# Kernel optimization log

Hardware: AMD Instinct MI355X
Metric: run time of the kernel (lower is better)

The kernel has to match this reference:

```python
import jax, jax.numpy as jnp
import numpy as np

DIM = 2048   # token width; == heads*head_dim
H, DH = 16, 128
B, S = 1, 2048
E, K = 4, 2          # routed experts, top-k
HID = 5632           # per-expert SwiGLU hidden: round256(int(2*(4*DIM)/3))
HS = 2816            # shared expert hidden: round256(int(2*(2*DIM)/3))


def setup_inputs() -> dict:
    key = jax.random.key(0)
    ks = jax.random.split(key, 24)
    def g(i, shape, s=0.02):
        return jax.random.normal(ks[i], shape, dtype=jnp.float32) * s
    return {
        "image_tokens": jax.random.normal(ks[0], (B, S, DIM), dtype=jnp.float32),
        "adaln_input": jax.random.normal(ks[1], (B, DIM), dtype=jnp.float32),
        "W_ada": g(2, (DIM, 6 * DIM)), "b_ada": g(3, (6 * DIM,)),
        "Wq": g(4, (DIM, DIM)), "bq": g(5, (DIM,)),
        "Wk": g(6, (DIM, DIM)), "bk": g(7, (DIM,)),
        "Wv": g(8, (DIM, DIM)), "bv": g(9, (DIM,)),
        "q_rms_w": jnp.ones((DIM,), jnp.float32) + g(10, (DIM,)),
        "k_rms_w": jnp.ones((DIM,), jnp.float32) + g(11, (DIM,)),
        "Wo": g(12, (DIM, DIM)), "bo": g(13, (DIM,)),
        "gate_w": g(14, (E, DIM)),
        "We1": g(15, (E, DIM, HID)), "We3": g(16, (E, DIM, HID)), "We2": g(17, (E, HID, DIM)),
        "Ws1": g(18, (DIM, HS)), "Ws3": g(19, (DIM, HS)), "Ws2": g(20, (HS, DIM)),
    }


def _ln(x):  # LayerNorm, elementwise_affine=False, eps=1e-6
    m = jnp.mean(x, -1, keepdims=True)
    v = jnp.var(x, -1, keepdims=True)
    return (x - m) * jax.lax.rsqrt(v + 1e-6)


def _rms(x, w):  # RMSNorm with affine weight, eps=1e-5
    return x * jax.lax.rsqrt(jnp.mean(x * x, -1, keepdims=True) + 1e-5) * w


def reference(image_tokens, adaln_input, W_ada, b_ada, Wq, bq, Wk, bk, Wv, bv,
              q_rms_w, k_rms_w, Wo, bo, gate_w, We1, We3, We2, Ws1, Ws3, Ws2):
    # adaLN: SiLU -> Linear -> 6 chunks, each broadcast as [B,1,dim]
    mod = (jax.nn.silu(adaln_input) @ W_ada + b_ada)[:, None, :]
    sh_msa, sc_msa, g_msa, sh_mlp, sc_mlp, g_mlp = jnp.split(mod, 6, axis=-1)

    # attention branch
    x = _ln(image_tokens) * (1.0 + sc_msa) + sh_msa
    q = _rms(x @ Wq + bq, q_rms_w).reshape(B, S, H, DH)
    k = _rms(x @ Wk + bk, k_rms_w).reshape(B, S, H, DH)
    v = (x @ Wv + bv).reshape(B, S, H, DH)
    att = jax.nn.softmax(jnp.einsum('bihd,bjhd->bhij', q, k) / jnp.sqrt(jnp.float32(DH)), axis=-1)
    o = jnp.einsum('bhij,bjhd->bihd', att, v).reshape(B, S, DIM) @ Wo + bo
    img = g_msa * o + image_tokens

    # MoE SwiGLU FFN branch
    y = _ln(img) * (1.0 + sc_mlp) + sh_mlp
    xf = y.reshape(-1, DIM)                                   # [N, dim]
    scores = jax.nn.softmax(xf @ gate_w.T, axis=-1)           # [N, E]
    tw, ti = jax.lax.top_k(scores, K)                         # no top-k renorm (norm_topk_prob=False)
    comb = jnp.zeros((xf.shape[0], E), xf.dtype).at[jnp.arange(xf.shape[0])[:, None], ti].add(tw)
    h = jax.nn.silu(jnp.einsum('nd,edh->neh', xf, We1)) * jnp.einsum('nd,edh->neh', xf, We3)
    routed = jnp.einsum('neh,ehd,ne->nd', h, We2, comb)
    shared = (jax.nn.silu(xf @ Ws1) * (xf @ Ws3)) @ Ws2
    ff = (routed + shared).reshape(B, S, DIM)

    return g_mlp * ff + img
```

## Files before the change

kernel.cpp:

```cpp
#include <hip/hip_runtime.h>
#include <hip/hip_bf16.h>

typedef unsigned short u16;
typedef __bf16 bf16x8 __attribute__((ext_vector_type(8)));
typedef float f32x4 __attribute__((ext_vector_type(4)));
typedef unsigned short u16x8 __attribute__((ext_vector_type(8)));

constexpr int DIMC = 2048;
constexpr int SEQ = 2048;
constexpr int NHEAD = 16;
constexpr int HDIM = 128;
constexpr int NEXP = 4;
constexpr int HIDC = 5632;
constexpr int HSH = 2816;
constexpr int MOD6 = 6 * DIMC;
constexpr int RSTRIDE = 2304;

static __device__ __forceinline__ u16 f2bf(float f) {
  __hip_bfloat16 b = __float2bfloat16(f);
  return __builtin_bit_cast(u16, b);
}
static __device__ __forceinline__ float bf2f(u16 u) {
  unsigned int x = ((unsigned int)u) << 16;
  return __builtin_bit_cast(float, x);
}
static __device__ __forceinline__ float sigf(float x) { return 1.f / (1.f + __expf(-x)); }

static __device__ __forceinline__ void gload16(const void* src, void* dst) {
  __builtin_amdgcn_global_load_lds((const __attribute__((address_space(1))) void*)src,
                                   (__attribute__((address_space(3))) void*)dst, 16, 0, 0);
}

static __device__ __forceinline__ void split44(f32x4 lo, f32x4 hi, bf16x8& h, bf16x8& l) {
#pragma unroll
  for (int e = 0; e < 4; ++e) {
    float f0 = lo[e];
    u16 h0 = f2bf(f0);
    h[e] = __builtin_bit_cast(__bf16, h0);
    l[e] = __builtin_bit_cast(__bf16, f2bf(f0 - bf2f(h0)));
    float f1 = hi[e];
    u16 h1 = f2bf(f1);
    h[4 + e] = __builtin_bit_cast(__bf16, h1);
    l[4 + e] = __builtin_bit_cast(__bf16, f2bf(f1 - bf2f(h1)));
  }
}

static __device__ __forceinline__ float blockSum(float v) {
#pragma unroll
  for (int m = 1; m < 64; m <<= 1) v += __shfl_xor(v, m);
  __shared__ float s[4];
  int w = threadIdx.x >> 6;
  if ((threadIdx.x & 63) == 0) s[w] = v;
  __syncthreads();
  float r = s[0] + s[1] + s[2] + s[3];
  __syncthreads();
  return r;
}

__global__ __launch_bounds__(256) void k_transpose(const float* __restrict__ in, u16* __restrict__ out,
                                                   int R, int C, int ldin, size_t inz, size_t outz) {
  __shared__ __align__(16) float tile[32][33];
  const float* inp = in + (size_t)blockIdx.z * inz;
  u16* outp = out + (size_t)blockIdx.z * outz;
  int tx = threadIdx.x & 31, ty = threadIdx.x >> 5;
  int c0 = blockIdx.x * 32, r0 = blockIdx.y * 32;
#pragma unroll
  for (int i = 0; i < 32; i += 8)
    tile[ty + i][tx] = inp[(size_t)(r0 + ty + i) * ldin + c0 + tx];
  __syncthreads();
#pragma unroll
  for (int i = 0; i < 32; i += 8)
    outp[(size_t)(c0 + ty + i) * R + r0 + tx] = f2bf(tile[tx][ty + i]);
}

__global__ __launch_bounds__(256) void k_transpose_f(const float* __restrict__ in, float* __restrict__ out,
                                                     int R, int C, int ldin) {
  __shared__ __align__(16) float tile[32][33];
  int tx = threadIdx.x & 31, ty = threadIdx.x >> 5;
  int c0 = blockIdx.x * 32, r0 = blockIdx.y * 32;
#pragma unroll
  for (int i = 0; i < 32; i += 8)
    tile[ty + i][tx] = in[(size_t)(r0 + ty + i) * ldin + c0 + tx];
  __syncthreads();
#pragma unroll
  for (int i = 0; i < 32; i += 8)
    out[(size_t)(c0 + ty + i) * R + r0 + tx] = tile[tx][ty + i];
}

__global__ __launch_bounds__(256) void k_adaln_p(const float* __restrict__ a, const float* __restrict__ W,
                                                 float* __restrict__ partial) {
  __shared__ float sa[128];
  int tid = threadIdx.x, slice = blockIdx.y;
  if (tid < 128) { float v = a[slice * 128 + tid]; sa[tid] = v * sigf(v); }
  __syncthreads();
  int j = blockIdx.x * 256 + tid;
  float acc = 0.f;
#pragma unroll 4
  for (int d = 0; d < 128; ++d) acc += sa[d] * W[(size_t)(slice * 128 + d) * MOD6 + j];
  partial[(size_t)slice * MOD6 + j] = acc;
}
__global__ __launch_bounds__(256) void k_adaln_r(const float* __restrict__ partial, const float* __restrict__ b,
                                                 float* __restrict__ mod) {
  int j = blockIdx.x * 256 + threadIdx.x;
  float acc = b[j];
#pragma unroll
  for (int s = 0; s < 16; ++s) acc += partial[(size_t)s * MOD6 + j];
  mod[j] = acc;
}

__global__ __launch_bounds__(256) void k_ln_modf(const float* __restrict__ X, const float* __restrict__ mod,
                                                 int shOff, int scOff, float* __restrict__ out) {
  int row = blockIdx.x, tid = threadIdx.x;
  const float4* x4 = (const float4*)(X + (size_t)row * DIMC);
  float4 v0 = x4[tid * 2], v1 = x4[tid * 2 + 1];
  float s = v0.x + v0.y + v0.z + v0.w + v1.x + v1.y + v1.z + v1.w;
  float ss = v0.x * v0.x + v0.y * v0.y + v0.z * v0.z + v0.w * v0.w +
             v1.x * v1.x + v1.y * v1.y + v1.z * v1.z + v1.w * v1.w;
  s = blockSum(s);
  ss = blockSum(ss);
  float mean = s * (1.f / DIMC);
  float var = ss * (1.f / DIMC) - mean * mean;
  float rstd = rsqrtf(var + 1e-6f);
  const float* sh = mod + shOff;
  const float* sc = mod + scOff;
  int c = tid * 8;
  float xv[8] = {v0.x, v0.y, v0.z, v0.w, v1.x, v1.y, v1.z, v1.w};
  float ov[8];
#pragma unroll
  for (int e = 0; e < 8; ++e) ov[e] = (xv[e] - mean) * rstd * (1.f + sc[c + e]) + sh[c + e];
  float4 o0 = {ov[0], ov[1], ov[2], ov[3]}, o1 = {ov[4], ov[5], ov[6], ov[7]};
  float4* y4 = (float4*)(out + (size_t)row * DIMC);
  y4[tid * 2] = o0;
  y4[tid * 2 + 1] = o1;
}

__global__ __launch_bounds__(256) void k_ln_mod(const float* __restrict__ X, const float* __restrict__ mod,
                                                int shOff, int scOff, u16* __restrict__ out) {
  int row = blockIdx.x, tid = threadIdx.x;
  const float4* x4 = (const float4*)(X + (size_t)row * DIMC);
  float4 v0 = x4[tid * 2], v1 = x4[tid * 2 + 1];
  float s = v0.x + v0.y + v0.z + v0.w + v1.x + v1.y + v1.z + v1.w;
  float ss = v0.x * v0.x + v0.y * v0.y + v0.z * v0.z + v0.w * v0.w +
             v1.x * v1.x + v1.y * v1.y + v1.z * v1.z + v1.w * v1.w;
  s = blockSum(s);
  ss = blockSum(ss);
  float mean = s * (1.f / DIMC);
  float var = ss * (1.f / DIMC) - mean * mean;
  float rstd = rsqrtf(var + 1e-6f);
  const float* sh = mod + shOff;
  const float* sc = mod + scOff;
  int c = tid * 8;
  float xv[8] = {v0.x, v0.y, v0.z, v0.w, v1.x, v1.y, v1.z, v1.w};
  u16x8 o;
#pragma unroll
  for (int e = 0; e < 8; ++e) o[e] = f2bf((xv[e] - mean) * rstd * (1.f + sc[c + e]) + sh[c + e]);
  *(u16x8*)(out + (size_t)row * DIMC + c) = o;
}

__global__ __launch_bounds__(256) void k_rms_f32(const float* __restrict__ X, const float* __restrict__ w,
                                                 float scale, float* __restrict__ out) {
  int row = blockIdx.x, tid = threadIdx.x;
  const float4* x4 = (const float4*)(X + (size_t)row * DIMC);
  float4 v0 = x4[tid * 2], v1 = x4[tid * 2 + 1];
  float ss = v0.x * v0.x + v0.y * v0.y + v0.z * v0.z + v0.w * v0.w +
             v1.x * v1.x + v1.y * v1.y + v1.z * v1.z + v1.w * v1.w;
  ss = blockSum(ss);
  float rstd = rsqrtf(ss * (1.f / DIMC) + 1e-5f) * scale;
  int c = tid * 8;
  float xv[8] = {v0.x, v0.y, v0.z, v0.w, v1.x, v1.y, v1.z, v1.w};
  float ov[8];
#pragma unroll
  for (int e = 0; e < 8; ++e) ov[e] = xv[e] * rstd * w[c + e];
  float4 o0 = {ov[0], ov[1], ov[2], ov[3]}, o1 = {ov[4], ov[5], ov[6], ov[7]};
  float4* y4 = (float4*)(out + (size_t)row * DIMC);
  y4[tid * 2] = o0;
  y4[tid * 2 + 1] = o1;
}

__global__ __launch_bounds__(256) void k_gate(const float* __restrict__ img, const float* __restrict__ mod,
                                              const float* __restrict__ gw, float* __restrict__ comb) {
  int n = blockIdx.x, tid = threadIdx.x;
  const float4* x4 = (const float4*)(img + (size_t)n * DIMC);
  float4 v0 = x4[tid * 2], v1 = x4[tid * 2 + 1];
  float s = v0.x + v0.y + v0.z + v0.w + v1.x + v1.y + v1.z + v1.w;
  float ss = v0.x * v0.x + v0.y * v0.y + v0.z * v0.z + v0.w * v0.w +
             v1.x * v1.x + v1.y * v1.y + v1.z * v1.z + v1.w * v1.w;
  s = blockSum(s);
  ss = blockSum(ss);
  float mean = s * (1.f / DIMC);
  float var = ss * (1.f / DIMC) - mean * mean;
  float rstd = rsqrtf(var + 1e-6f);
  const float* sh = mod + 3 * DIMC;
  const float* sc = mod + 4 * DIMC;
  int c = tid * 8;
  float xv[8] = {v0.x, v0.y, v0.z, v0.w, v1.x, v1.y, v1.z, v1.w};
  float y[8];
#pragma unroll
  for (int e = 0; e < 8; ++e) y[e] = (xv[e] - mean) * rstd * (1.f + sc[c + e]) + sh[c + e];
  float accs[NEXP];
#pragma unroll
  for (int ex = 0; ex < NEXP; ++ex) {
    float a = 0.f;
#pragma unroll
    for (int e = 0; e < 8; ++e) a += y[e] * gw[(size_t)ex * DIMC + c + e];
    accs[ex] = blockSum(a);
  }
  if (tid == 0) {
    float mx = fmaxf(fmaxf(accs[0], accs[1]), fmaxf(accs[2], accs[3]));
    float ex0 = __expf(accs[0] - mx), ex1 = __expf(accs[1] - mx);
    float ex2 = __expf(accs[2] - mx), ex3 = __expf(accs[3] - mx);
    float inv = 1.f / (ex0 + ex1 + ex2 + ex3);
    float v[4] = {ex0 * inv, ex1 * inv, ex2 * inv, ex3 * inv};
    int i1 = 0;
    for (int e = 1; e < 4; ++e)
      if (v[e] > v[i1]) i1 = e;
    int i2 = -1;
    for (int e = 0; e < 4; ++e) {
      if (e == i1) continue;
      if (i2 < 0 || v[e] > v[i2]) i2 = e;
    }
    for (int e = 0; e < 4; ++e) comb[(size_t)n * 4 + e] = (e == i1 || e == i2) ? v[e] : 0.f;
  }
}

__global__ __launch_bounds__(256) void k_route(const float* __restrict__ comb, int* __restrict__ gidx,
                                               float* __restrict__ cw, int* __restrict__ Mpad) {
  int wid = threadIdx.x >> 6, lane = threadIdx.x & 63;
  int base = 0;
  for (int c = 0; c < SEQ; c += 64) {
    int n = c + lane;
    float w = comb[(size_t)n * NEXP + wid];
    bool sel = w > 0.f;
    unsigned long long mask = __ballot(sel);
    int pos = __popcll(mask & ((1ull << lane) - 1ull));
    if (sel) {
      gidx[wid * RSTRIDE + base + pos] = n;
      cw[wid * RSTRIDE + base + pos] = w;
    }
    base += __popcll(mask);
  }
  int padded = (base + 127) & ~127;
  for (int i = base + lane; i < padded; i += 64) {
    gidx[wid * RSTRIDE + i] = -1;
    cw[wid * RSTRIDE + i] = 0.f;
  }
  if (lane == 0) Mpad[wid] = padded;
}

template <int MODE>
__global__ __launch_bounds__(256, 2) void k_gemm(const u16* __restrict__ A, const u16* __restrict__ BT,
                                                 int M, int N, int K, float* __restrict__ Cf,
                                                 u16* __restrict__ Cb, const u16* __restrict__ h1) {
  __shared__ __align__(16) u16 AsA[4096], AsB[4096], BsA[4096], BsB[4096];
  const int tid = threadIdx.x, wid = tid >> 6, lane = tid & 63;
  const int l16 = lane & 15, g = lane >> 4;
  const int wr = wid >> 1, wc = wid & 1;
  const int m0 = blockIdx.y * 128, n0 = blockIdx.x * 128;
  const int srow = lane >> 2, scol = (lane & 3) * 8;
  const u16* aS0 = A + (size_t)(m0 + wid * 32 + srow) * K + scol;
// ... 100 lines not shown
    row0 = slot0;
    row1 = slot0 + 16;
  } else {
    int t0 = gidxE[slot0], t1 = gidxE[slot0 + 16];
    row0 = t0 < 0 ? 0 : t0;
    row1 = t1 < 0 ? 0 : t1;
  }
  const u16* aS0 = A + (size_t)row0 * K + scol;
  const u16* aS1 = A + (size_t)row1 * K + scol;
  const u16* bS0 = BT + (size_t)(n0 + wid * 32 + srow) * K + scol;
  const u16* bS1 = bS0 + (size_t)16 * K;
  u16* aDA0 = &AsA[wid * 1024];
  u16* aDA1 = aDA0 + 512;
  u16* bDA0 = &BsA[wid * 1024];
  u16* bDA1 = bDA0 + 512;
  u16* aDB0 = &AsB[wid * 1024];
  u16* aDB1 = aDB0 + 512;
  u16* bDB0 = &BsB[wid * 1024];
  u16* bDB1 = bDB0 + 512;

  const f32x4 zero4 = {0.f, 0.f, 0.f, 0.f};
  f32x4 acc[4][4];
#pragma unroll
  for (int mi = 0; mi < 4; ++mi)
#pragma unroll
    for (int ni = 0; ni < 4; ++ni) acc[mi][ni] = zero4;

  for (int k0 = 0; k0 < K; k0 += 64) {
    __syncthreads();
    gload16(aS0 + k0, aDA0);
    gload16(aS1 + k0, aDA1);
    gload16(bS0 + k0, bDA0);
    gload16(bS1 + k0, bDA1);
    gload16(aS0 + k0 + 32, aDB0);
    gload16(aS1 + k0 + 32, aDB1);
    gload16(bS0 + k0 + 32, bDB0);
    gload16(bS1 + k0 + 32, bDB1);
    __syncthreads();
#pragma unroll
    for (int hh = 0; hh < 2; ++hh) {
      const u16* Asrc = hh ? AsB : AsA;
      const u16* Bsrc = hh ? BsB : BsA;
      bf16x8 af[4], bfr[4];
#pragma unroll
      for (int mi = 0; mi < 4; ++mi)
        af[mi] = *(const bf16x8*)(&Asrc[(wr * 64 + mi * 16 + l16) * 32 + g * 8]);
#pragma unroll
      for (int ni = 0; ni < 4; ++ni)
        bfr[ni] = *(const bf16x8*)(&Bsrc[(wc * 64 + ni * 16 + l16) * 32 + g * 8]);
#pragma unroll
      for (int mi = 0; mi < 4; ++mi)
#pragma unroll
        for (int ni = 0; ni < 4; ++ni)
          acc[mi][ni] = __builtin_amdgcn_mfma_f32_16x16x32_bf16(af[mi], bfr[ni], acc[mi][ni], 0, 0, 0);
    }
  }

#pragma unroll
  for (int mi = 0; mi < 4; ++mi) {
#pragma unroll
    for (int ni = 0; ni < 4; ++ni) {
      const int col = n0 + wc * 64 + ni * 16 + l16;
#pragma unroll
      for (int r = 0; r < 4; ++r) {
        const int slot = m0 + wr * 64 + mi * 16 + g * 4 + r;
        const size_t idx = (size_t)slot * N + col;
        float v = acc[mi][ni][r];
        if constexpr (RM == 0) {
          Cb[idx] = f2bf(v);
        } else if constexpr (RM == 1) {
          float hv = bf2f(h1[idx]);
          float sw = hv * sigf(hv);
          Cb[idx] = f2bf(sw * v * cwE[slot]);
        } else {
          int t = gidxE[slot];
          if (t >= 0) ff[(size_t)t * N + col] += v;
        }
      }
    }
  }
}

template <int MODE>
__global__ __launch_bounds__(256, 2) void k_gemm3(const float* __restrict__ A, const float* __restrict__ BT,
                                                  int M, int N, int K, float* __restrict__ Cf,
                                                  const float* __restrict__ bias,
                                                  const float* __restrict__ gvec,
                                                  const float* __restrict__ resid) {
  __shared__ __align__(16) u16 Ah[128 * 40], Al[128 * 40], Bh[128 * 40], Bl[128 * 40];
  const int tid = threadIdx.x, wid = tid >> 6, lane = tid & 63;
  const int l16 = lane & 15, g = lane >> 4;
  const int wr = wid >> 1, wc = wid & 1;
  const int m0 = blockIdx.y * 128, n0 = blockIdx.x * 128;

  const int srow = tid >> 1, se0 = (tid & 1) * 16;
  char* ahp = (char*)Ah + srow * 80 + se0 * 2;
  char* alp = (char*)Al + srow * 80 + se0 * 2;
  char* bhp = (char*)Bh + srow * 80 + se0 * 2;
  char* blp = (char*)Bl + srow * 80 + se0 * 2;
  const float* aS = A + (size_t)(m0 + srow) * K + se0;
  const float* bS = BT + (size_t)(n0 + srow) * K + se0;

  f32x4 ar[4], br[4];
#pragma unroll
  for (int c = 0; c < 4; ++c) {
    ar[c] = *(const f32x4*)(aS + c * 4);
    br[c] = *(const f32x4*)(bS + c * 4);
  }

  const f32x4 zero4 = {0.f, 0.f, 0.f, 0.f};
  f32x4 acc[4][4];
#pragma unroll
  for (int mi = 0; mi < 4; ++mi)
#pragma unroll
    for (int ni = 0; ni < 4; ++ni) acc[mi][ni] = zero4;

  for (int k0 = 0; k0 < K; k0 += 32) {
    __syncthreads();
    bf16x8 h0, l0, h1, l1;
    split44(ar[0], ar[1], h0, l0);
    split44(ar[2], ar[3], h1, l1);
    *(bf16x8*)(ahp) = h0;
    *(bf16x8*)(ahp + 16) = h1;
    *(bf16x8*)(alp) = l0;
    *(bf16x8*)(alp + 16) = l1;
    split44(br[0], br[1], h0, l0);
    split44(br[2], br[3], h1, l1);
    *(bf16x8*)(bhp) = h0;
    *(bf16x8*)(bhp + 16) = h1;
    *(bf16x8*)(blp) = l0;
    *(bf16x8*)(blp + 16) = l1;
    __syncthreads();
    if (k0 + 32 < K) {
#pragma unroll
      for (int c = 0; c < 4; ++c) {
        ar[c] = *(const f32x4*)(aS + k0 + 32 + c * 4);
        br[c] = *(const f32x4*)(bS + k0 + 32 + c * 4);
      }
    }
    bf16x8 bhf[4], blf[4];
#pragma unroll
    for (int ni = 0; ni < 4; ++ni) {
      const int rb = wc * 64 + ni * 16 + l16;
      bhf[ni] = *(const bf16x8*)((char*)Bh + rb * 80 + g * 16);
      blf[ni] = *(const bf16x8*)((char*)Bl + rb * 80 + g * 16);
    }
#pragma unroll
    for (int mi = 0; mi < 4; ++mi) {
      const int ra = wr * 64 + mi * 16 + l16;
      bf16x8 ahf = *(const bf16x8*)((char*)Ah + ra * 80 + g * 16);
      bf16x8 alf = *(const bf16x8*)((char*)Al + ra * 80 + g * 16);
#pragma unroll
      for (int ni = 0; ni < 4; ++ni) {
        acc[mi][ni] = __builtin_amdgcn_mfma_f32_16x16x32_bf16(alf, bhf[ni], acc[mi][ni], 0, 0, 0);
        acc[mi][ni] = __builtin_amdgcn_mfma_f32_16x16x32_bf16(ahf, blf[ni], acc[mi][ni], 0, 0, 0);
        acc[mi][ni] = __builtin_amdgcn_mfma_f32_16x16x32_bf16(ahf, bhf[ni], acc[mi][ni], 0, 0, 0);
      }
    }
  }

#pragma unroll
  for (int mi = 0; mi < 4; ++mi) {
#pragma unroll
    for (int ni = 0; ni < 4; ++ni) {
      const int col = n0 + wc * 64 + ni * 16 + l16;
      float bv = bias ? bias[col] : 0.f;
#pragma unroll
      for (int r = 0; r < 4; ++r) {
        const int row = m0 + wr * 64 + mi * 16 + g * 4 + r;
        float v = acc[mi][ni][r] + bv;
        if constexpr (MODE == 0) {
          Cf[(size_t)row * N + col] = v;
        } else if constexpr (MODE == 2) {
          Cf[(size_t)row * N + col] = v * gvec[col] + resid[(size_t)row * N + col];
        } else {
          Cf[(size_t)col * M + row] = v;
        }
      }
    }
  }
}

__global__ __launch_bounds__(256, 2) void k_flash3(const float* __restrict__ q, const float* __restrict__ kk,
                                                   const float* __restrict__ vt, float* __restrict__ o) {
  __shared__ __align__(16) u16 Kh[4096], Kl[4096], Vh[128 * 40], Vl[128 * 40];
  __shared__ __align__(16) u16 Pah[4][16 * 40], Pal[4][16 * 40];
  const int tid = threadIdx.x, wid = tid >> 6, lane = tid & 63;
  const int l16 = lane & 15, g = lane >> 4;
  const int h = blockIdx.y;
  const int r0 = blockIdx.x * 64 + wid * 16;
  const size_t hOff = (size_t)h * HDIM;

  bf16x8 qh[4], ql[4];
#pragma unroll
  for (int kc = 0; kc < 4; ++kc) {
    const float* qp = q + (size_t)(r0 + l16) * DIMC + hOff + kc * 32 + g * 8;
    split44(*(const f32x4*)qp, *(const f32x4*)(qp + 4), qh[kc], ql[kc]);
  }

  const int kr = tid >> 3, ke0 = (tid & 7) * 16;
  const int kswz = (kr & 7) << 4;
  const int kc0 = (ke0 * 2) ^ kswz, kc1 = (ke0 * 2 + 16) ^ kswz;
  char* khp = (char*)Kh + kr * 256;
  char* klp = (char*)Kl + kr * 256;
  const float* kBase = kk + (size_t)kr * DIMC + hOff + ke0;
  const int vr = tid >> 1, ve0 = (tid & 1) * 16;
  char* vhp = (char*)Vh + vr * 80 + ve0 * 2;
  char* vlp = (char*)Vl + vr * 80 + ve0 * 2;
  const float* vBase = vt + (size_t)(hOff + vr) * SEQ + ve0;

  f32x4 kReg[4], vReg[4];
#pragma unroll
  for (int c = 0; c < 4; ++c) {
    kReg[c] = *(const f32x4*)(kBase + c * 4);
    vReg[c] = *(const f32x4*)(vBase + c * 4);
  }

  const f32x4 zero4 = {0.f, 0.f, 0.f, 0.f};
  f32x4 oacc[8];
#pragma unroll
  for (int db = 0; db < 8; ++db) oacc[db] = zero4;
  float mr[4], lr[4];
#pragma unroll
  for (int r = 0; r < 4; ++r) {
    mr[r] = -3.0e38f;
    lr[r] = 0.f;
  }

  for (int j0 = 0; j0 < SEQ; j0 += 32) {
    __syncthreads();
    bf16x8 h0, l0, h1, l1;
    split44(kReg[0], kReg[1], h0, l0);
    split44(kReg[2], kReg[3], h1, l1);
    *(bf16x8*)(khp + kc0) = h0;
    *(bf16x8*)(khp + kc1) = h1;
    *(bf16x8*)(klp + kc0) = l0;
    *(bf16x8*)(klp + kc1) = l1;
    split44(vReg[0], vReg[1], h0, l0);
    split44(vReg[2], vReg[3], h1, l1);
    *(bf16x8*)(vhp) = h0;
    *(bf16x8*)(vhp + 16) = h1;
    *(bf16x8*)(vlp) = l0;
    *(bf16x8*)(vlp + 16) = l1;
    __syncthreads();
    if (j0 + 32 < SEQ) {
      const float* kp = kBase + (size_t)(j0 + 32) * DIMC;
      const float* vp = vBase + j0 + 32;
#pragma unroll
      for (int c = 0; c < 4; ++c) {
        kReg[c] = *(const f32x4*)(kp + c * 4);
        vReg[c] = *(const f32x4*)(vp + c * 4);
      }
    }
    f32x4 s0 = zero4, s1 = zero4;
    __builtin_amdgcn_s_setprio(1);
#pragma unroll
    for (int kc = 0; kc < 4; ++kc) {
      const int cb = (kc * 64 + g * 16) ^ ((l16 & 7) << 4);
      bf16x8 kh0 = *(const bf16x8*)((char*)Kh + l16 * 256 + cb);
      bf16x8 kl0 = *(const bf16x8*)((char*)Kl + l16 * 256 + cb);
      bf16x8 kh1 = *(const bf16x8*)((char*)Kh + (16 + l16) * 256 + cb);
      bf16x8 kl1 = *(const bf16x8*)((char*)Kl + (16 + l16) * 256 + cb);
      s0 = __builtin_amdgcn_mfma_f32_16x16x32_bf16(ql[kc], kh0, s0, 0, 0, 0);
      s0 = __builtin_amdgcn_mfma_f32_16x16x32_bf16(qh[kc], kl0, s0, 0, 0, 0);
      s0 = __builtin_amdgcn_mfma_f32_16x16x32_bf16(qh[kc], kh0, s0, 0, 0, 0);
      s1 = __builtin_amdgcn_mfma_f32_16x16x32_bf16(ql[kc], kh1, s1, 0, 0, 0);
      s1 = __builtin_amdgcn_mfma_f32_16x16x32_bf16(qh[kc], kl1, s1, 0, 0, 0);
      s1 = __builtin_amdgcn_mfma_f32_16x16x32_bf16(qh[kc], kh1, s1, 0, 0, 0);
    }
    __builtin_amdgcn_s_setprio(0);
    float corr[4];
#pragma unroll
    for (int r = 0; r < 4; ++r) {
      float tm = fmaxf(s0[r], s1[r]);
#pragma unroll
      for (int m = 1; m < 16; m <<= 1) tm = fmaxf(tm, __shfl_xor(tm, m));
      float mn = fmaxf(mr[r], tm);
      corr[r] = __expf(mr[r] - mn);
      mr[r] = mn;
      float p0 = __expf(s0[r] - mn);
      float p1 = __expf(s1[r] - mn);
      lr[r] = lr[r] * corr[r] + p0 + p1;
      u16 p0h = f2bf(p0), p1h = f2bf(p1);
      Pah[wid][(g * 4 + r) * 40 + l16] = p0h;
      Pah[wid][(g * 4 + r) * 40 + 16 + l16] = p1h;
      Pal[wid][(g * 4 + r) * 40 + l16] = f2bf(p0 - bf2f(p0h));
      Pal[wid][(g * 4 + r) * 40 + 16 + l16] = f2bf(p1 - bf2f(p1h));
    }
#pragma unroll
    for (int db = 0; db < 8; ++db)
#pragma unroll
      for (int r = 0; r < 4; ++r) oacc[db][r] *= corr[r];
    bf16x8 pfh = *(const bf16x8*)(&Pah[wid][l16 * 40 + g * 8]);
    bf16x8 pfl = *(const bf16x8*)(&Pal[wid][l16 * 40 + g * 8]);
    __builtin_amdgcn_s_setprio(1);
#pragma unroll
    for (int db = 0; db < 8; ++db) {
      const int row = db * 16 + l16;
      bf16x8 vh = *(const bf16x8*)((char*)Vh + row * 80 + g * 16);
      bf16x8 vl = *(const bf16x8*)((char*)Vl + row * 80 + g * 16);
      oacc[db] = __builtin_amdgcn_mfma_f32_16x16x32_bf16(pfl, vh, oacc[db], 0, 0, 0);
      oacc[db] = __builtin_amdgcn_mfma_f32_16x16x32_bf16(pfh, vl, oacc[db], 0, 0, 0);
      oacc[db] = __builtin_amdgcn_mfma_f32_16x16x32_bf16(pfh, vh, oacc[db], 0, 0, 0);
    }
    __builtin_amdgcn_s_setprio(0);
  }
#pragma unroll
  for (int r = 0; r < 4; ++r) {
#pragma unroll
    for (int m = 1; m < 16; m <<= 1) lr[r] += __shfl_xor(lr[r], m);
    lr[r] = 1.f / lr[r];
  }
#pragma unroll
  for (int db = 0; db < 8; ++db)
#pragma unroll
    for (int r = 0; r < 4; ++r)
      o[(size_t)(r0 + g * 4 + r) * DIMC + hOff + db * 16 + l16] = oacc[db][r] * lr[r];
}

__global__ __launch_bounds__(256) void k_final(const float* __restrict__ ff, const float* img,
                                               const float* __restrict__ mod, float* out) {
  const float4* gm = (const float4*)(mod + 5 * DIMC);
  const int total = SEQ * DIMC / 4;
  const int stride = gridDim.x * blockDim.x;
  for (int i = blockIdx.x * blockDim.x + threadIdx.x; i < total; i += stride) {
    int col4 = i & (DIMC / 4 - 1);
    float4 gv = gm[col4];
    float4 fv = ((const float4*)ff)[i];
    float4 iv = ((const float4*)img)[i];
    float4 ov;
    ov.x = gv.x * fv.x + iv.x;
    ov.y = gv.y * fv.y + iv.y;
    ov.z = gv.z * fv.z + iv.z;
    ov.w = gv.w * fv.w + iv.w;
    ((float4*)out)[i] = ov;
  }
}

extern "C" void kernel_launch(void* const* d_in, const int* in_sizes, int n_in, void* d_out, int out_size,
                              void* d_ws, size_t ws_size, hipStream_t stream) {
  (void)in_sizes; (void)n_in; (void)out_size; (void)ws_size;
  const float* image_tokens = (const float*)d_in[0];
  const float* adaln_input = (const float*)d_in[1];
  const float* W_ada = (const float*)d_in[2];
  const float* b_ada = (const float*)d_in[3];
  const float* Wq = (const float*)d_in[4];
  const float* bq = (const float*)d_in[5];
  const float* Wk = (const float*)d_in[6];
  const float* bk = (const float*)d_in[7];
  const float* Wv = (const float*)d_in[8];
  const float* bv = (const float*)d_in[9];
  const float* q_rms_w = (const float*)d_in[10];
  const float* k_rms_w = (const float*)d_in[11];
  const float* Wo = (const float*)d_in[12];
  const float* bo = (const float*)d_in[13];
  const float* gate_w = (const float*)d_in[14];
  const float* We1 = (const float*)d_in[15];
  const float* We3 = (const float*)d_in[16];
  const float* We2 = (const float*)d_in[17];
  const float* Ws1 = (const float*)d_in[18];
  const float* Ws3 = (const float*)d_in[19];
  const float* Ws2 = (const float*)d_in[20];

  char* cur = (char*)d_ws;
  auto alloc = [&](size_t n) {
    char* p = cur;
    cur += (n + 255) & ~(size_t)255;
    return p;
  };
  float* modv = (float*)alloc((size_t)MOD6 * 4);
  float* adap = (float*)alloc((size_t)16 * MOD6 * 4);
  float* comb = (float*)alloc((size_t)SEQ * NEXP * 4);
  int* gidx = (int*)alloc((size_t)NEXP * RSTRIDE * 4);
  float* cw = (float*)alloc((size_t)NEXP * RSTRIDE * 4);
  int* Mpad = (int*)alloc((size_t)NEXP * 4);
  float* xf = (float*)alloc((size_t)SEQ * DIMC * 4);
  float* wTf = (float*)alloc((size_t)DIMC * DIMC * 4);
  float* tf = (float*)alloc((size_t)SEQ * DIMC * 4);
  float* qf = (float*)alloc((size_t)SEQ * DIMC * 4);
  float* kf = (float*)alloc((size_t)SEQ * DIMC * 4);
  float* vtf = (float*)alloc((size_t)SEQ * DIMC * 4);
  float* aof = (float*)alloc((size_t)SEQ * DIMC * 4);
  u16* x_act = (u16*)alloc((size_t)SEQ * DIMC * 2);
  float* ff = (float*)alloc((size_t)SEQ * DIMC * 4);
  float* img = (float*)d_out;
  u16* wbufE = (u16*)xf;
  u16* H1G2 = (u16*)((char*)xf + (size_t)2 * HIDC * DIMC * 2);
  const size_t BZ = (size_t)HIDC * DIMC;
  const size_t CZ = (size_t)RSTRIDE * HIDC;
  u16* wbufS = wbufE;
  u16* H1Gs = H1G2;

  dim3 blk(256);
  auto gemm3 = [&](int mode, const float* A, const float* BT, int M, int N, int K, float* Cf,
                   const float* bias, const float* gv, const float* resid) {
    dim3 grid(N / 128, M / 128);
    switch (mode) {
      case 0: k_gemm3<0><<<grid, blk, 0, stream>>>(A, BT, M, N, K, Cf, bias, gv, resid); break;
      case 2: k_gemm3<2><<<grid, blk, 0, stream>>>(A, BT, M, N, K, Cf, bias, gv, resid); break;
      default: k_gemm3<6><<<grid, blk, 0, stream>>>(A, BT, M, N, K, Cf, bias, gv, resid); break;
    }
  };

  k_adaln_p<<<dim3(MOD6 / 256, 16), blk, 0, stream>>>(adaln_input, W_ada, adap);
  k_adaln_r<<<dim3(MOD6 / 256), blk, 0, stream>>>(adap, b_ada, modv);

  k_ln_modf<<<dim3(SEQ), blk, 0, stream>>>(image_tokens, modv, 0, DIMC, xf);
  k_transpose_f<<<dim3(DIMC / 32, DIMC / 32), blk, 0, stream>>>(Wq, wTf, DIMC, DIMC, DIMC);
  gemm3(0, xf, wTf, SEQ, DIMC, DIMC, tf, bq, nullptr, nullptr);
  k_rms_f32<<<dim3(SEQ), blk, 0, stream>>>(tf, q_rms_w, 0.08838834764831845f, qf);
  k_transpose_f<<<dim3(DIMC / 32, DIMC / 32), blk, 0, stream>>>(Wk, wTf, DIMC, DIMC, DIMC);
  gemm3(0, xf, wTf, SEQ, DIMC, DIMC, tf, bk, nullptr, nullptr);
  k_rms_f32<<<dim3(SEQ), blk, 0, stream>>>(tf, k_rms_w, 1.f, kf);
  k_transpose_f<<<dim3(DIMC / 32, DIMC / 32), blk, 0, stream>>>(Wv, wTf, DIMC, DIMC, DIMC);
  gemm3(6, xf, wTf, SEQ, DIMC, DIMC, vtf, bv, nullptr, nullptr);
  k_flash3<<<dim3(SEQ / 64, NHEAD), blk, 0, stream>>>(qf, kf, vtf, aof);
  k_transpose_f<<<dim3(DIMC / 32, DIMC / 32), blk, 0, stream>>>(Wo, wTf, DIMC, DIMC, DIMC);
  gemm3(2, aof, wTf, SEQ, DIMC, DIMC, img, bo, modv + 2 * DIMC, image_tokens);

  k_ln_mod<<<dim3(SEQ), blk, 0, stream>>>(img, modv, 3 * DIMC, 4 * DIMC, x_act);
  k_gate<<<dim3(SEQ), blk, 0, stream>>>(img, modv, gate_w, comb);
  k_route<<<dim3(1), blk, 0, stream>>>(comb, gidx, cw, Mpad);

  k_transpose<<<dim3(HSH / 32, DIMC / 32), blk, 0, stream>>>(Ws1, wbufS, DIMC, HSH, HSH, 0, 0);
  k_gemm<1><<<dim3(HSH / 128, SEQ / 128), blk, 0, stream>>>(x_act, wbufS, SEQ, HSH, DIMC, nullptr,
                                                            H1Gs, nullptr);
  k_transpose<<<dim3(HSH / 32, DIMC / 32), blk, 0, stream>>>(Ws3, wbufS, DIMC, HSH, HSH, 0, 0);
  k_gemm<3><<<dim3(HSH / 128, SEQ / 128), blk, 0, stream>>>(x_act, wbufS, SEQ, HSH, DIMC, nullptr,
                                                            H1Gs, H1Gs);
  k_transpose<<<dim3(DIMC / 32, HSH / 32), blk, 0, stream>>>(Ws2, wbufS, HSH, DIMC, DIMC, 0, 0);
  k_gemm<0><<<dim3(DIMC / 128, SEQ / 128), blk, 0, stream>>>(H1Gs, wbufS, SEQ, DIMC, HSH, ff,
                                                             nullptr, nullptr);

  const size_t WE = (size_t)DIMC * HIDC;
  for (int p = 0; p < 2; ++p) {
    const int e0 = p * 2;
    const int* ge = gidx + e0 * RSTRIDE;
    const float* ce = cw + e0 * RSTRIDE;
    const int* me = Mpad + e0;
    k_transpose<<<dim3(HIDC / 32, DIMC / 32, 2), blk, 0, stream>>>(We1 + (size_t)e0 * WE, wbufE,
                                                                   DIMC, HIDC, HIDC, WE, BZ);
    k_gemmR<0><<<dim3(HIDC / 128, SEQ / 128, 2), blk, 0, stream>>>(x_act, 0, wbufE, BZ, HIDC, DIMC,
                                                                   ge, ce, me, H1G2, CZ, H1G2, nullptr);
    k_transpose<<<dim3(HIDC / 32, DIMC / 32, 2), blk, 0, stream>>>(We3 + (size_t)e0 * WE, wbufE,
                                                                   DIMC, HIDC, HIDC, WE, BZ);
    k_gemmR<1><<<dim3(HIDC / 128, SEQ / 128, 2), blk, 0, stream>>>(x_act, 0, wbufE, BZ, HIDC, DIMC,
                                                                   ge, ce, me, H1G2, CZ, H1G2, nullptr);
    k_transpose<<<dim3(DIMC / 32, HIDC / 32, 2), blk, 0, stream>>>(We2 + (size_t)e0 * WE, wbufE,
                                                                   HIDC, DIMC, DIMC, WE, BZ);
    for (int z = 0; z < 2; ++z) {
      k_gemmR<2><<<dim3(DIMC / 128, SEQ / 128, 1), blk, 0, stream>>>(
          H1G2 + (size_t)z * CZ, 0, wbufE + (size_t)z * BZ, 0, DIMC, HIDC, gidx + (e0 + z) * RSTRIDE,
          cw + (e0 + z) * RSTRIDE, Mpad + e0 + z, H1G2, 0, H1G2, ff);
    }
  }

  k_final<<<dim3(1024), blk, 0, stream>>>(ff, img, modv, (float*)d_out);
}
```

Measured before the change: 1.694 ms.

## Pre-split fp32 operands into bf16 hi/lo pairs in producer kernels for attention GEMMs

```diff
diff --git a/kernel.cpp b/kernel.cpp
--- a/kernel.cpp
+++ b/kernel.cpp
@@ -25,24 +25,14 @@
   return __builtin_bit_cast(float, x);
 }
 static __device__ __forceinline__ float sigf(float x) { return 1.f / (1.f + __expf(-x)); }
+static __device__ __forceinline__ void splitf(float f, u16& h, u16& l) {
+  h = f2bf(f);
+  l = f2bf(f - bf2f(h));
+}
 
 static __device__ __forceinline__ void gload16(const void* src, void* dst) {
   __builtin_amdgcn_global_load_lds((const __attribute__((address_space(1))) void*)src,
                                    (__attribute__((address_space(3))) void*)dst, 16, 0, 0);
-}
-
-static __device__ __forceinline__ void split44(f32x4 lo, f32x4 hi, bf16x8& h, bf16x8& l) {
-#pragma unroll
-  for (int e = 0; e < 4; ++e) {
-    float f0 = lo[e];
-    u16 h0 = f2bf(f0);
-    h[e] = __builtin_bit_cast(__bf16, h0);
-    l[e] = __builtin_bit_cast(__bf16, f2bf(f0 - bf2f(h0)));
-    float f1 = hi[e];
-    u16 h1 = f2bf(f1);
-    h[4 + e] = __builtin_bit_cast(__bf16, h1);
-    l[4 + e] = __builtin_bit_cast(__bf16, f2bf(f1 - bf2f(h1)));
-  }
 }
 
 static __device__ __forceinline__ float blockSum(float v) {
@@ -73,8 +63,8 @@
     outp[(size_t)(c0 + ty + i) * R + r0 + tx] = f2bf(tile[tx][ty + i]);
 }
 
-__global__ __launch_bounds__(256) void k_transpose_f(const float* __restrict__ in, float* __restrict__ out,
-                                                     int R, int C, int ldin) {
+__global__ __launch_bounds__(256) void k_transpose_s(const float* __restrict__ in, u16* __restrict__ outh,
+                                                     u16* __restrict__ outl, int R, int C, int ldin) {
   __shared__ __align__(16) float tile[32][33];
   int tx = threadIdx.x & 31, ty = threadIdx.x >> 5;
   int c0 = blockIdx.x * 32, r0 = blockIdx.y * 32;
@@ -83,8 +73,14 @@
     tile[ty + i][tx] = in[(size_t)(r0 + ty + i) * ldin + c0 + tx];
   __syncthreads();
 #pragma unroll
-  for (int i = 0; i < 32; i += 8)
-    out[(size_t)(c0 + ty + i) * R + r0 + tx] = tile[tx][ty + i];
+  for (int i = 0; i < 32; i += 8) {
+    float v = tile[tx][ty + i];
+    u16 h, l;
+    splitf(v, h, l);
+    size_t idx = (size_t)(c0 + ty + i) * R + r0 + tx;
+    outh[idx] = h;
+    outl[idx] = l;
+  }
 }
 
 __global__ __launch_bounds__(256) void k_adaln_p(const float* __restrict__ a, const float* __restrict__ W,
@@ -108,8 +104,9 @@
   mod[j] = acc;
 }
 
-__global__ __launch_bounds__(256) void k_ln_modf(const float* __restrict__ X, const float* __restrict__ mod,
-                                                 int shOff, int scOff, float* __restrict__ out) {
+__global__ __launch_bounds__(256) void k_ln_mod_split(const float* __restrict__ X, const float* __restrict__ mod,
+                                                      int shOff, int scOff, u16* __restrict__ outh,
+                                                      u16* __restrict__ outl) {
   int row = blockIdx.x, tid = threadIdx.x;
   const float4* x4 = (const float4*)(X + (size_t)row * DIMC);
   float4 v0 = x4[tid * 2], v1 = x4[tid * 2 + 1];
@@ -125,13 +122,17 @@
   const float* sc = mod + scOff;
   int c = tid * 8;
   float xv[8] = {v0.x, v0.y, v0.z, v0.w, v1.x, v1.y, v1.z, v1.w};
-  float ov[8];
-#pragma unroll
-  for (int e = 0; e < 8; ++e) ov[e] = (xv[e] - mean) * rstd * (1.f + sc[c + e]) + sh[c + e];
-  float4 o0 = {ov[0], ov[1], ov[2], ov[3]}, o1 = {ov[4], ov[5], ov[6], ov[7]};
-  float4* y4 = (float4*)(out + (size_t)row * DIMC);
-  y4[tid * 2] = o0;
-  y4[tid * 2 + 1] = o1;
+  u16x8 oh, ol;
+#pragma unroll
+  for (int e = 0; e < 8; ++e) {
+    float v = (xv[e] - mean) * rstd * (1.f + sc[c + e]) + sh[c + e];
+    u16 h, l;
+    splitf(v, h, l);
+    oh[e] = h;
+    ol[e] = l;
+  }
+  *(u16x8*)(outh + (size_t)row * DIMC + c) = oh;
+  *(u16x8*)(outl + (size_t)row * DIMC + c) = ol;
 }
 
 __global__ __launch_bounds__(256) void k_ln_mod(const float* __restrict__ X, const float* __restrict__ mod,
@@ -157,8 +158,9 @@
   *(u16x8*)(out + (size_t)row * DIMC + c) = o;
 }
 
-__global__ __launch_bounds__(256) void k_rms_f32(const float* __restrict__ X, const float* __restrict__ w,
-                                                 float scale, float* __restrict__ out) {
+__global__ __launch_bounds__(256) void k_rms_split(const float* __restrict__ X, const float* __restrict__ w,
+                                                   float scale, u16* __restrict__ outh,
+                                                   u16* __restrict__ outl) {
   int row = blockIdx.x, tid = threadIdx.x;
   const float4* x4 = (const float4*)(X + (size_t)row * DIMC);
   float4 v0 = x4[tid * 2], v1 = x4[tid * 2 + 1];
@@ -168,13 +170,17 @@
   float rstd = rsqrtf(ss * (1.f / DIMC) + 1e-5f) * scale;
   int c = tid * 8;
   float xv[8] = {v0.x, v0.y, v0.z, v0.w, v1.x, v1.y, v1.z, v1.w};
-  float ov[8];
-#pragma unroll
-  for (int e = 0; e < 8; ++e) ov[e] = xv[e] * rstd * w[c + e];
-  float4 o0 = {ov[0], ov[1], ov[2], ov[3]}, o1 = {ov[4], ov[5], ov[6], ov[7]};
-  float4* y4 = (float4*)(out + (size_t)row * DIMC);
-  y4[tid * 2] = o0;
-  y4[tid * 2 + 1] = o1;
+  u16x8 oh, ol;
+#pragma unroll
+  for (int e = 0; e < 8; ++e) {
+    float v = xv[e] * rstd * w[c + e];
+    u16 h, l;
+    splitf(v, h, l);
+    oh[e] = h;
+    ol[e] = l;
+  }
+  *(u16x8*)(outh + (size_t)row * DIMC + c) = oh;
+  *(u16x8*)(outl + (size_t)row * DIMC + c) = ol;
 }
 
 __global__ __launch_bounds__(256) void k_gate(const float* __restrict__ img, const float* __restrict__ mod,
@@ -441,31 +447,31 @@
 }
 
 template <int MODE>
-__global__ __launch_bounds__(256, 2) void k_gemm3(const float* __restrict__ A, const float* __restrict__ BT,
-                                                  int M, int N, int K, float* __restrict__ Cf,
-                                                  const float* __restrict__ bias,
-                                                  const float* __restrict__ gvec,
-                                                  const float* __restrict__ resid) {
-  __shared__ __align__(16) u16 Ah[128 * 40], Al[128 * 40], Bh[128 * 40], Bl[128 * 40];
+__global__ __launch_bounds__(256, 3) void k_gemm3s(const u16* __restrict__ Ahg, const u16* __restrict__ Alg,
+                                                   const u16* __restrict__ Bhg, const u16* __restrict__ Blg,
+                                                   int M, int N, int K, float* __restrict__ Cf,
+                                                   u16* __restrict__ Ch, u16* __restrict__ Cl,
+                                                   const float* __restrict__ bias,
+                                                   const float* __restrict__ gvec,
+                                                   const float* __restrict__ resid) {
+  __shared__ __align__(16) u16 Ahs[4096], Als[4096], Bhs[4096], Bls[4096];
   const int tid = threadIdx.x, wid = tid >> 6, lane = tid & 63;
   const int l16 = lane & 15, g = lane >> 4;
   const int wr = wid >> 1, wc = wid & 1;
   const int m0 = blockIdx.y * 128, n0 = blockIdx.x * 128;
-
-  const int srow = tid >> 1, se0 = (tid & 1) * 16;
-  char* ahp = (char*)Ah + srow * 80 + se0 * 2;
-  char* alp = (char*)Al + srow * 80 + se0 * 2;
-  char* bhp = (char*)Bh + srow * 80 + se0 * 2;
-  char* blp = (char*)Bl + srow * 80 + se0 * 2;
-  const float* aS = A + (size_t)(m0 + srow) * K + se0;
-  const float* bS = BT + (size_t)(n0 + srow) * K + se0;
-
-  f32x4 ar[4], br[4];
-#pragma unroll
-  for (int c = 0; c < 4; ++c) {
-    ar[c] = *(const f32x4*)(aS + c * 4);
-    br[c] = *(const f32x4*)(bS + c * 4);
-  }
+  const int srow = lane >> 2, scol = (lane & 3) * 8;
+  const size_t aOff0 = (size_t)(m0 + wid * 32 + srow) * K + scol;
+  const size_t aOff1 = aOff0 + (size_t)16 * K;
+  const size_t bOff0 = (size_t)(n0 + wid * 32 + srow) * K + scol;
+  const size_t bOff1 = bOff0 + (size_t)16 * K;
+  u16* dA0 = wid * 1024 + Ahs;
+  u16* dA1 = dA0 + 512;
+  u16* dAl0 = wid * 1024 + Als;
+  u16* dAl1 = dAl0 + 512;
+  u16* dB0 = wid * 1024 + Bhs;
+  u16* dB1 = dB0 + 512;
+  u16* dBl0 = wid * 1024 + Bls;
+  u16* dBl1 = dBl0 + 512;
 
   const f32x4 zero4 = {0.f, 0.f, 0.f, 0.f};
   f32x4 acc[4][4];
@@ -476,39 +482,25 @@
 
   for (int k0 = 0; k0 < K; k0 += 32) {
     __syncthreads();
-    bf16x8 h0, l0, h1, l1;
-    split44(ar[0], ar[1], h0, l0);
-    split44(ar[2], ar[3], h1, l1);
-    *(bf16x8*)(ahp) = h0;
-    *(bf16x8*)(ahp + 16) = h1;
-    *(bf16x8*)(alp) = l0;
-    *(bf16x8*)(alp + 16) = l1;
-    split44(br[0], br[1], h0, l0);
-    split44(br[2], br[3], h1, l1);
-    *(bf16x8*)(bhp) = h0;
-    *(bf16x8*)(bhp + 16) = h1;
-    *(bf16x8*)(blp) = l0;
-    *(bf16x8*)(blp + 16) = l1;
+    gload16(Ahg + aOff0 + k0, dA0);
+    gload16(Ahg + aOff1 + k0, dA1);
+    gload16(Alg + aOff0 + k0, dAl0);
+    gload16(Alg + aOff1 + k0, dAl1);
+    gload16(Bhg + bOff0 + k0, dB0);
+    gload16(Bhg + bOff1 + k0, dB1);
+    gload16(Blg + bOff0 + k0, dBl0);
+    gload16(Blg + bOff1 + k0, dBl1);
     __syncthreads();
-    if (k0 + 32 < K) {
-#pragma unroll
-      for (int c = 0; c < 4; ++c) {
-        ar[c] = *(const f32x4*)(aS + k0 + 32 + c * 4);
-        br[c] = *(const f32x4*)(bS + k0 + 32 + c * 4);
-      }
-    }
     bf16x8 bhf[4], blf[4];
 #pragma unroll
     for (int ni = 0; ni < 4; ++ni) {
-      const int rb = wc * 64 + ni * 16 + l16;
-      bhf[ni] = *(const bf16x8*)((char*)Bh + rb * 80 + g * 16);
-      blf[ni] = *(const bf16x8*)((char*)Bl + rb * 80 + g * 16);
+      bhf[ni] = *(const bf16x8*)(&Bhs[(wc * 64 + ni * 16 + l16) * 32 + g * 8]);
+      blf[ni] = *(const bf16x8*)(&Bls[(wc * 64 + ni * 16 + l16) * 32 + g * 8]);
     }
 #pragma unroll
     for (int mi = 0; mi < 4; ++mi) {
-      const int ra = wr * 64 + mi * 16 + l16;
-      bf16x8 ahf = *(const bf16x8*)((char*)Ah + ra * 80 + g * 16);
-      bf16x8 alf = *(const bf16x8*)((char*)Al + ra * 80 + g * 16);
+      bf16x8 ahf = *(const bf16x8*)(&Ahs[(wr * 64 + mi * 16 + l16) * 32 + g * 8]);
+      bf16x8 alf = *(const bf16x8*)(&Als[(wr * 64 + mi * 16 + l16) * 32 + g * 8]);
 #pragma unroll
       for (int ni = 0; ni < 4; ++ni) {
         acc[mi][ni] = __builtin_amdgcn_mfma_f32_16x16x32_bf16(alf, bhf[ni], acc[mi][ni], 0, 0, 0);
@@ -533,15 +525,20 @@
         } else if constexpr (MODE == 2) {
           Cf[(size_t)row * N + col] = v * gvec[col] + resid[(size_t)row * N + col];
         } else {
-          Cf[(size_t)col * M + row] = v;
+          u16 h, l;
+          splitf(v, h, l);
+          Ch[(size_t)col * M + row] = h;
+          Cl[(size_t)col * M + row] = l;
         }
       }
     }
   }
 }
 
-__global__ __launch_bounds__(256, 2) void k_flash3(const float* __restrict__ q, const float* __restrict__ kk,
-                                                   const float* __restrict__ vt, float* __restrict__ o) {
+__global__ __launch_bounds__(256, 3) void k_flash3(const u16* __restrict__ qh_g, const u16* __restrict__ ql_g,
+                                                   const u16* __restrict__ kh_g, const u16* __restrict__ kl_g,
+                                                   const u16* __restrict__ vth_g, const u16* __restrict__ vtl_g,
+                                                   u16* __restrict__ oh_g, u16* __restrict__ ol_g) {
   __shared__ __align__(16) u16 Kh[4096], Kl[4096], Vh[128 * 40], Vl[128 * 40];
   __shared__ __align__(16) u16 Pah[4][16 * 40], Pal[4][16 * 40];
   const int tid = threadIdx.x, wid = tid >> 6, lane = tid & 63;
@@ -550,11 +547,12 @@
   const int r0 = blockIdx.x * 64 + wid * 16;
   const size_t hOff = (size_t)h * HDIM;
 
-  bf16x8 qh[4], ql[4];
+  bf16x8 qfh[4], qfl[4];
 #pragma unroll
   for (int kc = 0; kc < 4; ++kc) {
-    const float* qp = q + (size_t)(r0 + l16) * DIMC + hOff + kc * 32 + g * 8;
-    split44(*(const f32x4*)qp, *(const f32x4*)(qp + 4), qh[kc], ql[kc]);
+    const size_t qo = (size_t)(r0 + l16) * DIMC + hOff + kc * 32 + g * 8;
+    qfh[kc] = *(const bf16x8*)(qh_g + qo);
+    qfl[kc] = *(const bf16x8*)(ql_g + qo);
   }
 
   const int kr = tid >> 3, ke0 = (tid & 7) * 16;
@@ -562,18 +560,21 @@
   const int kc0 = (ke0 * 2) ^ kswz, kc1 = (ke0 * 2 + 16) ^ kswz;
   char* khp = (char*)Kh + kr * 256;
   char* klp = (char*)Kl + kr * 256;
-  const float* kBase = kk + (size_t)kr * DIMC + hOff + ke0;
+  const size_t kOff = (size_t)kr * DIMC + hOff + ke0;
   const int vr = tid >> 1, ve0 = (tid & 1) * 16;
   char* vhp = (char*)Vh + vr * 80 + ve0 * 2;
   char* vlp = (char*)Vl + vr * 80 + ve0 * 2;
-  const float* vBase = vt + (size_t)(hOff + vr) * SEQ + ve0;
-
-  f32x4 kReg[4], vReg[4];
-#pragma unroll
-  for (int c = 0; c < 4; ++c) {
-    kReg[c] = *(const f32x4*)(kBase + c * 4);
-    vReg[c] = *(const f32x4*)(vBase + c * 4);
-  }
+  const size_t vOff = (size_t)(hOff + vr) * SEQ + ve0;
+
+  u16x8 kH0, kH1, kL0, kL1, vH0, vH1, vL0, vL1;
+  kH0 = *(const u16x8*)(kh_g + kOff);
+  kH1 = *(const u16x8*)(kh_g + kOff + 8);
+  kL0 = *(const u16x8*)(kl_g + kOff);
+  kL1 = *(const u16x8*)(kl_g + kOff + 8);
+  vH0 = *(const u16x8*)(vth_g + vOff);
+  vH1 = *(const u16x8*)(vth_g + vOff + 8);
+  vL0 = *(const u16x8*)(vtl_g + vOff);
+  vL1 = *(const u16x8*)(vtl_g + vOff + 8);
 
   const f32x4 zero4 = {0.f, 0.f, 0.f, 0.f};
   f32x4 oacc[8];
@@ -588,28 +589,26 @@
 
   for (int j0 = 0; j0 < SEQ; j0 += 32) {
     __syncthreads();
-    bf16x8 h0, l0, h1, l1;
-    split44(kReg[0], kReg[1], h0, l0);
-    split44(kReg[2], kReg[3], h1, l1);
-    *(bf16x8*)(khp + kc0) = h0;
-    *(bf16x8*)(khp + kc1) = h1;
-    *(bf16x8*)(klp + kc0) = l0;
-    *(bf16x8*)(klp + kc1) = l1;
-    split44(vReg[0], vReg[1], h0, l0);
-    split44(vReg[2], vReg[3], h1, l1);
-    *(bf16x8*)(vhp) = h0;
-    *(bf16x8*)(vhp + 16) = h1;
-    *(bf16x8*)(vlp) = l0;
-    *(bf16x8*)(vlp + 16) = l1;
+    *(u16x8*)(khp + kc0) = kH0;
+    *(u16x8*)(khp + kc1) = kH1;
+    *(u16x8*)(klp + kc0) = kL0;
+    *(u16x8*)(klp + kc1) = kL1;
+    *(u16x8*)(vhp) = vH0;
+    *(u16x8*)(vhp + 16) = vH1;
+    *(u16x8*)(vlp) = vL0;
+    *(u16x8*)(vlp + 16) = vL1;
     __syncthreads();
     if (j0 + 32 < SEQ) {
-      const float* kp = kBase + (size_t)(j0 + 32) * DIMC;
-      const float* vp = vBase + j0 + 32;
-#pragma unroll
-      for (int c = 0; c < 4; ++c) {
-        kReg[c] = *(const f32x4*)(kp + c * 4);
-        vReg[c] = *(const f32x4*)(vp + c * 4);
-      }
+      const size_t ko = kOff + (size_t)(j0 + 32) * DIMC;
+      const size_t vo = vOff + j0 + 32;
+      kH0 = *(const u16x8*)(kh_g + ko);
+      kH1 = *(const u16x8*)(kh_g + ko + 8);
+      kL0 = *(const u16x8*)(kl_g + ko);
+      kL1 = *(const u16x8*)(kl_g + ko + 8);
+      vH0 = *(const u16x8*)(vth_g + vo);
+      vH1 = *(const u16x8*)(vth_g + vo + 8);
+      vL0 = *(const u16x8*)(vtl_g + vo);
+      vL1 = *(const u16x8*)(vtl_g + vo + 8);
     }
     f32x4 s0 = zero4, s1 = zero4;
     __builtin_amdgcn_s_setprio(1);
@@ -620,12 +619,12 @@
       bf16x8 kl0 = *(const bf16x8*)((char*)Kl + l16 * 256 + cb);
       bf16x8 kh1 = *(const bf16x8*)((char*)Kh + (16 + l16) * 256 + cb);
       bf16x8 kl1 = *(const bf16x8*)((char*)Kl + (16 + l16) * 256 + cb);
-      s0 = __builtin_amdgcn_mfma_f32_16x16x32_bf16(ql[kc], kh0, s0, 0, 0, 0);
-      s0 = __builtin_amdgcn_mfma_f32_16x16x32_bf16(qh[kc], kl0, s0, 0, 0, 0);
-      s0 = __builtin_amdgcn_mfma_f32_16x16x32_bf16(qh[kc], kh0, s0, 0, 0, 0);
-      s1 = __builtin_amdgcn_mfma_f32_16x16x32_bf16(ql[kc], kh1, s1, 0, 0, 0);
-      s1 = __builtin_amdgcn_mfma_f32_16x16x32_bf16(qh[kc], kl1, s1, 0, 0, 0);
-      s1 = __builtin_amdgcn_mfma_f32_16x16x32_bf16(qh[kc], kh1, s1, 0, 0, 0);
+      s0 = __builtin_amdgcn_mfma_f32_16x16x32_bf16(qfl[kc], kh0, s0, 0, 0, 0);
+      s0 = __builtin_amdgcn_mfma_f32_16x16x32_bf16(qfh[kc], kl0, s0, 0, 0, 0);
+      s0 = __builtin_amdgcn_mfma_f32_16x16x32_bf16(qfh[kc], kh0, s0, 0, 0, 0);
+      s1 = __builtin_amdgcn_mfma_f32_16x16x32_bf16(qfl[kc], kh1, s1, 0, 0, 0);
+      s1 = __builtin_amdgcn_mfma_f32_16x16x32_bf16(qfh[kc], kl1, s1, 0, 0, 0);
+      s1 = __builtin_amdgcn_mfma_f32_16x16x32_bf16(qfh[kc], kh1, s1, 0, 0, 0);
     }
     __builtin_amdgcn_s_setprio(0);
     float corr[4];
@@ -673,8 +672,14 @@
 #pragma unroll
   for (int db = 0; db < 8; ++db)
 #pragma unroll
-    for (int r = 0; r < 4; ++r)
-      o[(size_t)(r0 + g * 4 + r) * DIMC + hOff + db * 16 + l16] = oacc[db][r] * lr[r];
+    for (int r = 0; r < 4; ++r) {
+      float v = oacc[db][r] * lr[r];
+      u16 hh, ll;
+      splitf(v, hh, ll);
+      const size_t idx = (size_t)(r0 + g * 4 + r) * DIMC + hOff + db * 16 + l16;
+      oh_g[idx] = hh;
+      ol_g[idx] = ll;
+    }
 }
 
 __global__ __launch_bounds__(256) void k_final(const float* __restrict__ ff, const float* img,
@@ -733,49 +738,61 @@
   int* gidx = (int*)alloc((size_t)NEXP * RSTRIDE * 4);
   float* cw = (float*)alloc((size_t)NEXP * RSTRIDE * 4);
   int* Mpad = (int*)alloc((size_t)NEXP * 4);
-  float* xf = (float*)alloc((size_t)SEQ * DIMC * 4);
-  float* wTf = (float*)alloc((size_t)DIMC * DIMC * 4);
+  u16* xh = (u16*)alloc((size_t)SEQ * DIMC * 2);
+  u16* xl = (u16*)alloc((size_t)SEQ * DIMC * 2);
+  u16* wTh = (u16*)alloc((size_t)DIMC * DIMC * 2);
+  u16* wTl = (u16*)alloc((size_t)DIMC * DIMC * 2);
   float* tf = (float*)alloc((size_t)SEQ * DIMC * 4);
-  float* qf = (float*)alloc((size_t)SEQ * DIMC * 4);
-  float* kf = (float*)alloc((size_t)SEQ * DIMC * 4);
-  float* vtf = (float*)alloc((size_t)SEQ * DIMC * 4);
-  float* aof = (float*)alloc((size_t)SEQ * DIMC * 4);
+  u16* qhb = (u16*)alloc((size_t)SEQ * DIMC * 2);
+  u16* qlb = (u16*)alloc((size_t)SEQ * DIMC * 2);
+  u16* khb = (u16*)alloc((size_t)SEQ * DIMC * 2);
+  u16* klb = (u16*)alloc((size_t)SEQ * DIMC * 2);
+  u16* vth = (u16*)alloc((size_t)SEQ * DIMC * 2);
+  u16* vtl = (u16*)alloc((size_t)SEQ * DIMC * 2);
+  u16* aoh = (u16*)alloc((size_t)SEQ * DIMC * 2);
+  u16* aol = (u16*)alloc((size_t)SEQ * DIMC * 2);
   u16* x_act = (u16*)alloc((size_t)SEQ * DIMC * 2);
   float* ff = (float*)alloc((size_t)SEQ * DIMC * 4);
   float* img = (float*)d_out;
-  u16* wbufE = (u16*)xf;
-  u16* H1G2 = (u16*)((char*)xf + (size_t)2 * HIDC * DIMC * 2);
+  u16* wbufE = xh;
+  u16* H1G2 = (u16*)((char*)xh + (size_t)2 * HIDC * DIMC * 2);
   const size_t BZ = (size_t)HIDC * DIMC;
   const size_t CZ = (size_t)RSTRIDE * HIDC;
   u16* wbufS = wbufE;
   u16* H1Gs = H1G2;
 
   dim3 blk(256);
-  auto gemm3 = [&](int mode, const float* A, const float* BT, int M, int N, int K, float* Cf,
-                   const float* bias, const float* gv, const float* resid) {
+  auto gemm3s = [&](int mode, const u16* Ah, const u16* Al, int M, int N, int K, float* Cf, u16* Ch,
+                    u16* Cl, const float* bias, const float* gv, const float* resid) {
     dim3 grid(N / 128, M / 128);
     switch (mode) {
-      case 0: k_gemm3<0><<<grid, blk, 0, stream>>>(A, BT, M, N, K, Cf, bias, gv, resid); break;
-      case 2: k_gemm3<2><<<grid, blk, 0, stream>>>(A, BT, M, N, K, Cf, bias, gv, resid); break;
-      default: k_gemm3<6><<<grid, blk, 0, stream>>>(A, BT, M, N, K, Cf, bias, gv, resid); break;
+      case 0:
+        k_gemm3s<0><<<grid, blk, 0, stream>>>(Ah, Al, wTh, wTl, M, N, K, Cf, Ch, Cl, bias, gv, resid);
+        break;
+      case 2:
+        k_gemm3s<2><<<grid, blk, 0, stream>>>(Ah, Al, wTh, wTl, M, N, K, Cf, Ch, Cl, bias, gv, resid);
+        break;
+      default:
+        k_gemm3s<6><<<grid, blk, 0, stream>>>(Ah, Al, wTh, wTl, M, N, K, Cf, Ch, Cl, bias, gv, resid);
+        break;
     }
   };
 
   k_adaln_p<<<dim3(MOD6 / 256, 16), blk, 0, stream>>>(adaln_input, W_ada, adap);
   k_adaln_r<<<dim3(MOD6 / 256), blk, 0, stream>>>(adap, b_ada, modv);
 
-  k_ln_modf<<<dim3(SEQ), blk, 0, stream>>>(image_tokens, modv, 0, DIMC, xf);
-  k_transpose_f<<<dim3(DIMC / 32, DIMC / 32), blk, 0, stream>>>(Wq, wTf, DIMC, DIMC, DIMC);
-  gemm3(0, xf, wTf, SEQ, DIMC, DIMC, tf, bq, nullptr, nullptr);
-  k_rms_f32<<<dim3(SEQ), blk, 0, stream>>>(tf, q_rms_w, 0.08838834764831845f, qf);
-  k_transpose_f<<<dim3(DIMC / 32, DIMC / 32), blk, 0, stream>>>(Wk, wTf, DIMC, DIMC, DIMC);
-  gemm3(0, xf, wTf, SEQ, DIMC, DIMC, tf, bk, nullptr, nullptr);
-  k_rms_f32<<<dim3(SEQ), blk, 0, stream>>>(tf, k_rms_w, 1.f, kf);
-  k_transpose_f<<<dim3(DIMC / 32, DIMC / 32), blk, 0, stream>>>(Wv, wTf, DIMC, DIMC, DIMC);
-  gemm3(6, xf, wTf, SEQ, DIMC, DIMC, vtf, bv, nullptr, nullptr);
-  k_flash3<<<dim3(SEQ / 64, NHEAD), blk, 0, stream>>>(qf, kf, vtf, aof);
-  k_transpose_f<<<dim3(DIMC / 32, DIMC / 32), blk, 0, stream>>>(Wo, wTf, DIMC, DIMC, DIMC);
-  gemm3(2, aof, wTf, SEQ, DIMC, DIMC, img, bo, modv + 2 * DIMC, image_tokens);
+  k_ln_mod_split<<<dim3(SEQ), blk, 0, stream>>>(image_tokens, modv, 0, DIMC, xh, xl);
+  k_transpose_s<<<dim3(DIMC / 32, DIMC / 32), blk, 0, stream>>>(Wq, wTh, wTl, DIMC, DIMC, DIMC);
+  gemm3s(0, xh, xl, SEQ, DIMC, DIMC, tf, nullptr, nullptr, bq, nullptr, nullptr);
+  k_rms_split<<<dim3(SEQ), blk, 0, stream>>>(tf, q_rms_w, 0.08838834764831845f, qhb, qlb);
+  k_transpose_s<<<dim3(DIMC / 32, DIMC / 32), blk, 0, stream>>>(Wk, wTh, wTl, DIMC, DIMC, DIMC);
+  gemm3s(0, xh, xl, SEQ, DIMC, DIMC, tf, nullptr, nullptr, bk, nullptr, nullptr);
+  k_rms_split<<<dim3(SEQ), blk, 0, stream>>>(tf, k_rms_w, 1.f, khb, klb);
+  k_transpose_s<<<dim3(DIMC / 32, DIMC / 32), blk, 0, stream>>>(Wv, wTh, wTl, DIMC, DIMC, DIMC);
+  gemm3s(6, xh, xl, SEQ, DIMC, DIMC, nullptr, vth, vtl, bv, nullptr, nullptr);
+  k_flash3<<<dim3(SEQ / 64, NHEAD), blk, 0, stream>>>(qhb, qlb, khb, klb, vth, vtl, aoh, aol);
+  k_transpose_s<<<dim3(DIMC / 32, DIMC / 32), blk, 0, stream>>>(Wo, wTh, wTl, DIMC, DIMC, DIMC);
+  gemm3s(2, aoh, aol, SEQ, DIMC, DIMC, img, nullptr, nullptr, bo, modv + 2 * DIMC, image_tokens);
 
   k_ln_mod<<<dim3(SEQ), blk, 0, stream>>>(img, modv, 3 * DIMC, 4 * DIMC, x_act);
   k_gate<<<dim3(SEQ), blk, 0, stream>>>(img, modv, gate_w, comb);
```

After: 1.727 ms. Within noise of the previous version (+1.9%).
